# Kernel tuning notes

Hardware: AMD Instinct MI355X
Metric: run time of the kernel (lower is better)

## Reference

```python
import jax, jax.numpy as jnp
import numpy as np

B, N, D, K = 32, 2048, 512, 256
NEG_SLOPE = 0.01  # torch LeakyReLU default


def setup_inputs() -> dict:
    key = jax.random.key(0)
    k1, k2, k3, k4, k5, k6 = jax.random.split(key, 6)
    s = 1.0 / np.sqrt(D)
    sk = 1.0 / np.sqrt(K)
    return {
        "vI": jax.random.normal(k1, (B, N, D), dtype=jnp.float32),
        "vQ": jax.random.normal(k2, (B, D), dtype=jnp.float32),
        "Wi": jax.random.uniform(k3, (D, K), minval=-s, maxval=s, dtype=jnp.float32),
        "Wq": jax.random.uniform(k4, (D, K), minval=-s, maxval=s, dtype=jnp.float32),
        "bq": jax.random.uniform(k5, (K,), minval=-s, maxval=s, dtype=jnp.float32),
        "Wp": jax.random.uniform(k6, (K, 1), minval=-sk, maxval=sk, dtype=jnp.float32),
        "bp": jnp.zeros((1,), dtype=jnp.float32),
    }


def reference(vI, vQ, Wi, Wq, bq, Wp, bp):
    # vI: [B,N,D], vQ: [B,D]
    vIp = jnp.einsum("bnd,dk->bnk", vI, Wi)          # [B,N,K] (no bias)
    vQp = vQ @ Wq + bq                                  # [B,K]
    ha = jax.nn.leaky_relu(vIp + vQp[:, None, :], NEG_SLOPE)  # [B,N,K]
    scores = jnp.einsum("bnk,k->bn", ha, Wp[:, 0]) + bp[0]    # [B,N]
    pi = jax.nn.softmax(scores, axis=-1)                # [B,N]
    vI_attn = jnp.einsum("bn,bnk->bk", pi, vIp)        # [B,K]
    return vI_attn + vQp
```

## Files before the change

kernel.cpp:

```cpp
#include <hip/hip_runtime.h>

#define CB 32
#define CN 2048
#define CD 512
#define CK 256

typedef __bf16 bf16x8 __attribute__((ext_vector_type(8)));
typedef float  f32x4  __attribute__((ext_vector_type(4)));

__device__ __forceinline__ unsigned pk2bf(float a, float b) {
    union { float f; unsigned u; } x, y; x.f = a; y.f = b;
    unsigned ru = x.u + 0x7fffu + ((x.u >> 16) & 1u);
    unsigned rv = y.u + 0x7fffu + ((y.u >> 16) & 1u);
    return (ru >> 16) | (rv & 0xffff0000u);
}

__device__ __forceinline__ unsigned short bf16r(float a) {
    union { float f; unsigned u; } x; x.f = a;
    unsigned r = x.u + 0x7fffu + ((x.u >> 16) & 1u);
    return (unsigned short)(r >> 16);
}

__device__ __forceinline__ void glds16(const void* g, void* l) {
    __builtin_amdgcn_global_load_lds(
        (const __attribute__((address_space(1))) void*)g,
        (__attribute__((address_space(3))) void*)l, 16, 0, 0);
}

__global__ __launch_bounds__(256) void prep_kernel(
        const float* __restrict__ Wi, const float* __restrict__ Wq,
        const float* __restrict__ vQ, const float* __restrict__ bq,
        unsigned short* __restrict__ WiT, float* __restrict__ vQpP)
{
    const int tid = threadIdx.x;
    if (blockIdx.x < 32) {
        const int t = blockIdx.x;
        const int d0 = (t >> 2) * 64, k0 = (t & 3) * 64;
        __shared__ float sT[64][68];
        const int r = tid >> 4, c4 = (tid & 15) * 4;
        #pragma unroll
        for (int i = 0; i < 4; ++i) {
            float4 v = *reinterpret_cast<const float4*>(
                Wi + (size_t)(d0 + r + i * 16) * CK + k0 + c4);
            *reinterpret_cast<float4*>(&sT[r + i * 16][c4]) = v;
        }
        __syncthreads();
        const int k = tid >> 2, dg = (tid & 3) * 16;
        unsigned short __attribute__((aligned(16))) ov[16];
        #pragma unroll
        for (int j = 0; j < 16; ++j) ov[j] = bf16r(sT[dg + j][k]);
        unsigned short* dst = WiT + (size_t)(k0 + k) * CD + d0 + dg;
        *reinterpret_cast<uint4*>(dst)     = *reinterpret_cast<const uint4*>(&ov[0]);
        *reinterpret_cast<uint4*>(dst + 8) = *reinterpret_cast<const uint4*>(&ov[8]);
    } else {
        const int bb = blockIdx.x - 32;
        const int b = bb >> 3, j = bb & 7;
        __shared__ float sq[64];
        if (tid < 64) sq[tid] = vQ[b * CD + j * 64 + tid];
        __syncthreads();
        float acc = (j == 0) ? bq[tid] : 0.f;
        const float* wq = Wq + (size_t)j * 64 * CK + tid;
        #pragma unroll
        for (int d = 0; d < 64; d += 8) {
            float wv[8];
            #pragma unroll
            for (int u = 0; u < 8; ++u) wv[u] = wq[(d + u) * CK];
            #pragma unroll
            for (int u = 0; u < 8; ++u) acc += sq[d + u] * wv[u];
        }
        vQpP[(size_t)bb * CK + tid] = acc;
    }
}

__global__ __launch_bounds__(256, 2) void scores_fused_kernel(
        const float* __restrict__ vI, const unsigned short* __restrict__ WiT,
        const float* __restrict__ vQpP, const float* __restrict__ Wp,
        float* __restrict__ numP, float* __restrict__ Zp, float* __restrict__ mP)
{
    constexpr int BM = 128, BK = 64, LDA = BK + 8;
    __shared__ __align__(16) unsigned short sA[BM][LDA];
    __shared__ __align__(16) unsigned short sB[CK * BK];
    float* sred = (float*)sB;
    float* sS   = ((float*)sB) + 512;
    float* sW   = ((float*)sB) + 640;

    const int tid  = threadIdx.x;
    const int b    = blockIdx.y;
    const int n0   = blockIdx.x * BM;
    const int wave = tid >> 6;
    const int lane = tid & 63;
    const int col  = lane & 15;
    const int quad = lane >> 4;

    const float* vIb = vI + ((size_t)b * CN + n0) * CD;

    int gBoff[8];
    #pragma unroll
    for (int t = 0; t < 8; ++t) {
        int row = wave * 64 + t * 8 + (lane >> 3);
        int c   = (lane & 7) ^ (row & 7);
        gBoff[t] = row * CD + c * 8;
    }

    f32x4 acc[8][4];
    #pragma unroll
    for (int mt = 0; mt < 8; ++mt)
        #pragma unroll
        for (int kt = 0; kt < 4; ++kt)
            acc[mt][kt] = (f32x4){0.f, 0.f, 0.f, 0.f};

    const int ar = tid >> 4;
    const int ac = (tid & 15) * 4;

    for (int d0 = 0; d0 < CD; d0 += BK) {
        __syncthreads();
        #pragma unroll
        for (int t = 0; t < 8; ++t)
            glds16(WiT + gBoff[t] + d0, (unsigned short*)sB + (wave * 8 + t) * 512);
        #pragma unroll
        for (int i = 0; i < 8; ++i) {
            int r = ar + i * 16;
            float4 v = *reinterpret_cast<const float4*>(vIb + (size_t)r * CD + d0 + ac);
            uint2 p; p.x = pk2bf(v.x, v.y); p.y = pk2bf(v.z, v.w);
            *reinterpret_cast<uint2*>(&sA[r][ac]) = p;
        }
        __syncthreads();
        #pragma unroll
        for (int s = 0; s < 2; ++s) {
            const int dk = s * 32 + quad * 8;
            const int slot = (4 * s + quad) ^ (col & 7);
            bf16x8 af[8], bfr[4];
            #pragma unroll
            for (int mt = 0; mt < 8; ++mt)
                af[mt] = *reinterpret_cast<const bf16x8*>(&sA[mt * 16 + col][dk]);
            #pragma unroll
            for (int kt = 0; kt < 4; ++kt) {
                int R = wave * 64 + kt * 16 + col;
                bfr[kt] = *reinterpret_cast<const bf16x8*>(
                    (unsigned short*)sB + R * 64 + slot * 8);
            }
            #pragma unroll
            for (int mt = 0; mt < 8; ++mt)
                #pragma unroll
                for (int kt = 0; kt < 4; ++kt)
                    acc[mt][kt] = __builtin_amdgcn_mfma_f32_16x16x32_bf16(
                        af[mt], bfr[kt], acc[mt][kt], 0, 0, 0);
        }
    }

    float vq[4], wp[4];
    #pragma unroll
    for (int kt = 0; kt < 4; ++kt) {
        int k = wave * 64 + kt * 16 + col;
        float a = 0.f;
        #pragma unroll
        for (int j = 0; j < 8; ++j) a += vQpP[(b * 8 + j) * CK + k];
        vq[kt] = a;
        wp[kt] = Wp[k];
    }
    float sp[8][4];
    #pragma unroll
    for (int mt = 0; mt < 8; ++mt)
        #pragma unroll
        for (int r = 0; r < 4; ++r) {
            float s = 0.f;
            #pragma unroll
            for (int kt = 0; kt < 4; ++kt) {
                float v = acc[mt][kt][r] + vq[kt];
                v = v > 0.f ? v : 0.01f * v;
                s += v * wp[kt];
            }
            sp[mt][r] = s;
        }
    #pragma unroll
    for (int off = 1; off < 16; off <<= 1)
        #pragma unroll
        for (int mt = 0; mt < 8; ++mt)
            #pragma unroll
            for (int r = 0; r < 4; ++r)
                sp[mt][r] += __shfl_xor(sp[mt][r], off);

    __syncthreads();
    if (col == 0) {
        #pragma unroll
        for (int mt = 0; mt < 8; ++mt)
            #pragma unroll
            for (int r = 0; r < 4; ++r)
                sred[wave * 128 + mt * 16 + quad * 4 + r] = sp[mt][r];
    }
    __syncthreads();
    if (tid < BM)
        sS[tid] = sred[tid] + sred[128 + tid] + sred[256 + tid] + sred[384 + tid];
    __syncthreads();

    float m = -1e30f;
    #pragma unroll 8
    for (int i = 0; i < BM; ++i) m = fmaxf(m, sS[i]);
    if (tid < BM) sW[tid] = __expf(sS[tid] - m);
    __syncthreads();
    float z = (tid < BM) ? sW[tid] : 0.f;
    #pragma unroll
    for (int off = 32; off > 0; off >>= 1) z += __shfl_xor(z, off);
    if (lane == 0) sS[wave] = z;
    __syncthreads();
    const int pidx = b * 16 + blockIdx.x;
    if (tid == 0) {
        Zp[pidx] = sS[0] + sS[1] + sS[2] + sS[3];
        mP[pidx] = m;
    }

    float nk[4] = {0.f, 0.f, 0.f, 0.f};
    #pragma unroll
    for (int mt = 0; mt < 8; ++mt)
        #pragma unroll
        for (int r = 0; r < 4; ++r) {
            float w = sW[mt * 16 + quad * 4 + r];
            #pragma unroll
            for (int kt = 0; kt < 4; ++kt)
                nk[kt] += w * acc[mt][kt][r];
        }
    #pragma unroll
    for (int kt = 0; kt < 4; ++kt) {
        nk[kt] += __shfl_xor(nk[kt], 16);
        nk[kt] += __shfl_xor(nk[kt], 32);
    }
    if (quad == 0) {
        #pragma unroll
        for (int kt = 0; kt < 4; ++kt)
            numP[(size_t)pidx * CK + wave * 64 + kt * 16 + col] = nk[kt];
    }
}

__global__ __launch_bounds__(256) void finalize_kernel(
        const float* __restrict__ numP, const float* __restrict__ Zp,
        const float* __restrict__ mP, const float* __restrict__ vQpP,
        float* __restrict__ out)
{
    const int b = blockIdx.x, tid = threadIdx.x;
    float M = -1e30f;
    #pragma unroll
    for (int j = 0; j < 16; ++j) M = fmaxf(M, mP[b * 16 + j]);
    float w[16]; float Zt = 0.f;
    #pragma unroll
    for (int j = 0; j < 16; ++j) {
        w[j] = __expf(mP[b * 16 + j] - M);
        Zt += w[j] * Zp[b * 16 + j];
    }
    const float inv = 1.f / Zt;
    float s = 0.f;
    #pragma unroll
    for (int j = 0; j < 16; ++j) s += w[j] * numP[(size_t)(b * 16 + j) * CK + tid];
    float vq = 0.f;
    #pragma unroll
    for (int j = 0; j < 8; ++j) vq += vQpP[(size_t)(b * 8 + j) * CK + tid];
    out[b * CK + tid] = s * inv + vq;
}

extern "C" void kernel_launch(void* const* d_in, const int* in_sizes, int n_in,
                              void* d_out, int out_size, void* d_ws, size_t ws_size,
                              hipStream_t stream)
{
    const float* vI = (const float*)d_in[0];
    const float* vQ = (const float*)d_in[1];
    const float* Wi = (const float*)d_in[2];
    const float* Wq = (const float*)d_in[3];
    const float* bq = (const float*)d_in[4];
    const float* Wp = (const float*)d_in[5];
    float* out = (float*)d_out;

    char* ws = (char*)d_ws;
    float*          vQpP = (float*)(ws);
    unsigned short* WiT  = (unsigned short*)(ws + 262144);
    float*          numP = (float*)(ws + 524288);
    float*          Zp   = (float*)(ws + 524288 + 524288);
    float*          mP   = (float*)(ws + 1048576 + 2048);

    prep_kernel        <<<288, 256, 0, stream>>>(Wi, Wq, vQ, bq, WiT, vQpP);
    scores_fused_kernel<<<dim3(CN / 128, CB), 256, 0, stream>>>(vI, WiT, vQpP, Wp,
                                                                numP, Zp, mP);
    finalize_kernel    <<<CB, 256, 0, stream>>>(numP, Zp, mP, vQpP, out);
}
```

Before: 218.1 us.

## Load vI fragments directly into registers and double-buffer Wi tiles in LDS

The A operand (vI) is no longer staged through shared memory. Each lane loads its fp32 fragment straight from global memory and converts it to bf16 in registers just before the MFMA. The Wi tile is double-buffered in LDS so the next tile's async load overlaps the current compute, which cuts each iteration to one barrier. In exchange, every wave loads the same vI rows redundantly (4x across waves, relying on cache), and register pressure from the fp32 fragments rises.

```diff
diff --git a/kernel.cpp b/kernel.cpp
--- a/kernel.cpp
+++ b/kernel.cpp
@@ -77,12 +77,11 @@
         const float* __restrict__ vQpP, const float* __restrict__ Wp,
         float* __restrict__ numP, float* __restrict__ Zp, float* __restrict__ mP)
 {
-    constexpr int BM = 128, BK = 64, LDA = BK + 8;
-    __shared__ __align__(16) unsigned short sA[BM][LDA];
-    __shared__ __align__(16) unsigned short sB[CK * BK];
-    float* sred = (float*)sB;
-    float* sS   = ((float*)sB) + 512;
-    float* sW   = ((float*)sB) + 640;
+    constexpr int BM = 128, BK = 64;
+    __shared__ __align__(16) unsigned short sB[2][CK * BK];
+    float* sred = (float*)sB[0];
+    float* sS   = ((float*)sB[0]) + 512;
+    float* sW   = ((float*)sB[0]) + 640;
 
     const int tid  = threadIdx.x;
     const int b    = blockIdx.y;
@@ -92,7 +91,8 @@
     const int col  = lane & 15;
     const int quad = lane >> 4;
 
-    const float* vIb = vI + ((size_t)b * CN + n0) * CD;
+    const float* vIb   = vI + ((size_t)b * CN + n0) * CD;
+    const float* aBase = vIb + (size_t)col * CD + quad * 8;
 
     int gBoff[8];
     #pragma unroll
@@ -109,43 +109,59 @@
         for (int kt = 0; kt < 4; ++kt)
             acc[mt][kt] = (f32x4){0.f, 0.f, 0.f, 0.f};
 
-    const int ar = tid >> 4;
-    const int ac = (tid & 15) * 4;
-
-    for (int d0 = 0; d0 < CD; d0 += BK) {
-        __syncthreads();
-        #pragma unroll
-        for (int t = 0; t < 8; ++t)
-            glds16(WiT + gBoff[t] + d0, (unsigned short*)sB + (wave * 8 + t) * 512);
-        #pragma unroll
-        for (int i = 0; i < 8; ++i) {
-            int r = ar + i * 16;
-            float4 v = *reinterpret_cast<const float4*>(vIb + (size_t)r * CD + d0 + ac);
-            uint2 p; p.x = pk2bf(v.x, v.y); p.y = pk2bf(v.z, v.w);
-            *reinterpret_cast<uint2*>(&sA[r][ac]) = p;
-        }
-        __syncthreads();
+    #pragma unroll
+    for (int i = 0; i < 8; ++i)
+        glds16(WiT + gBoff[i], (unsigned short*)sB[0] + (wave * 8 + i) * 512);
+    __syncthreads();
+
+    for (int t = 0; t < 8; ++t) {
+        const int d0 = t * BK;
+        const unsigned short* bufC = sB[t & 1];
+
+        f32x4 a0[8], a1[8];
+        #pragma unroll
+        for (int mt = 0; mt < 8; ++mt) {
+            const float* p = aBase + (size_t)(mt * 16) * CD + d0;
+            a0[mt] = *reinterpret_cast<const f32x4*>(p);
+            a1[mt] = *reinterpret_cast<const f32x4*>(p + 4);
+        }
+        if (t < 7) {
+            #pragma unroll
+            for (int i = 0; i < 8; ++i)
+                glds16(WiT + gBoff[i] + d0 + BK,
+                       (unsigned short*)sB[(t + 1) & 1] + (wave * 8 + i) * 512);
+        }
         #pragma unroll
         for (int s = 0; s < 2; ++s) {
-            const int dk = s * 32 + quad * 8;
+            if (s == 1) {
+                #pragma unroll
+                for (int mt = 0; mt < 8; ++mt) {
+                    const float* p = aBase + (size_t)(mt * 16) * CD + d0 + 32;
+                    a0[mt] = *reinterpret_cast<const f32x4*>(p);
+                    a1[mt] = *reinterpret_cast<const f32x4*>(p + 4);
+                }
+            }
             const int slot = (4 * s + quad) ^ (col & 7);
-            bf16x8 af[8], bfr[4];
-            #pragma unroll
-            for (int mt = 0; mt < 8; ++mt)
-                af[mt] = *reinterpret_cast<const bf16x8*>(&sA[mt * 16 + col][dk]);
+            bf16x8 bfr[4];
             #pragma unroll
             for (int kt = 0; kt < 4; ++kt) {
                 int R = wave * 64 + kt * 16 + col;
-                bfr[kt] = *reinterpret_cast<const bf16x8*>(
-                    (unsigned short*)sB + R * 64 + slot * 8);
-            }
-            #pragma unroll
-            for (int mt = 0; mt < 8; ++mt)
+                bfr[kt] = *reinterpret_cast<const bf16x8*>(bufC + R * 64 + slot * 8);
+            }
+            #pragma unroll
+            for (int mt = 0; mt < 8; ++mt) {
+                union { unsigned u[4]; bf16x8 v; } af;
+                af.u[0] = pk2bf(a0[mt].x, a0[mt].y);
+                af.u[1] = pk2bf(a0[mt].z, a0[mt].w);
+                af.u[2] = pk2bf(a1[mt].x, a1[mt].y);
+                af.u[3] = pk2bf(a1[mt].z, a1[mt].w);
                 #pragma unroll
                 for (int kt = 0; kt < 4; ++kt)
                     acc[mt][kt] = __builtin_amdgcn_mfma_f32_16x16x32_bf16(
-                        af[mt], bfr[kt], acc[mt][kt], 0, 0, 0);
-        }
+                        af.v, bfr[kt], acc[mt][kt], 0, 0, 0);
+            }
+        }
+        __syncthreads();
     }
 
     float vq[4], wp[4];
```

Result: slower. 248.3 us (+13.9%).
